# Optimization experiments

Hardware: AMD Instinct MI355X
Metric: run time of the kernel (lower is better)

Reference implementation:

```python
import jax, jax.numpy as jnp
import numpy as np

B, T, D, H, V, K = 64, 128, 300, 256, 30000, 16
FILTERS = [3, 4, 5]
FN = [100, 100, 100]
CLS = 5


def setup_inputs() -> dict:
    key = jax.random.key(0)
    ks = jax.random.split(key, 32)
    n = lambda i, shape, s=0.05: (jax.random.normal(ks[i], shape, jnp.float32) * s)
    inp = jax.random.randint(ks[0], (B, T), 0, V)
    emb = n(1, (V + 2, D)).at[V + 1].set(0.0)  # padding_idx row = 0
    # GRU (1 layer, bidirectional), PyTorch gate order r,z,n
    Wx_f, Wh_f = n(2, (3 * H, D)), n(3, (3 * H, H))
    bx_f, bh_f = n(4, (3 * H,)), n(5, (3 * H,))
    Wx_b, Wh_b = n(6, (3 * H, D)), n(7, (3 * H, H))
    bx_b, bh_b = n(8, (3 * H,)), n(9, (3 * H,))
    fc1c_W, fc1c_b = n(10, (D, 2 * H)), n(11, (D,))
    concept_table = n(12, (V, K, D), 0.1)
    counts = jax.random.randint(ks[13], (V,), 1, K + 1)
    concept_mask = (jnp.arange(K)[None, :] < counts[:, None])  # bool [V,K]
    conv_W0, conv_b0 = n(14, (FN[0], FILTERS[0] * 2 * D)), n(15, (FN[0],))
    conv_W1, conv_b1 = n(16, (FN[1], FILTERS[1] * 2 * D)), n(17, (FN[1],))
    conv_W2, conv_b2 = n(18, (FN[2], FILTERS[2] * 2 * D)), n(19, (FN[2],))
    fc1_W, fc1_b = n(20, (100, sum(FN))), n(21, (100,))
    fc2_W, fc2_b = n(22, (CLS, 100)), n(23, (CLS,))
    return dict(inp=inp, emb=emb, Wx_f=Wx_f, Wh_f=Wh_f, bx_f=bx_f, bh_f=bh_f,
                Wx_b=Wx_b, Wh_b=Wh_b, bx_b=bx_b, bh_b=bh_b,
                fc1c_W=fc1c_W, fc1c_b=fc1c_b,
                concept_table=concept_table, concept_mask=concept_mask,
                conv_W0=conv_W0, conv_b0=conv_b0, conv_W1=conv_W1, conv_b1=conv_b1,
                conv_W2=conv_W2, conv_b2=conv_b2,
                fc1_W=fc1_W, fc1_b=fc1_b, fc2_W=fc2_W, fc2_b=fc2_b)


def _gru_dir(x, Wx, Wh, bx, bh):
    # x: [B,T,D] -> hidden states [B,T,H]; PyTorch GRU cell math.
    xg = jnp.einsum('btd,gd->btg', x, Wx) + bx  # precompute input gates [B,T,3H]

    def step(h, xg_t):
        gh = h @ Wh.T + bh
        xr, xz, xn = jnp.split(xg_t, 3, axis=-1)
        hr, hz, hn = jnp.split(gh, 3, axis=-1)
        r = jax.nn.sigmoid(xr + hr)
        z = jax.nn.sigmoid(xz + hz)
        nn_ = jnp.tanh(xn + r * hn)
        h2 = (1.0 - z) * nn_ + z * h
        return h2, h2

    h0 = jnp.zeros((x.shape[0], Wh.shape[1]), x.dtype)
    _, ys = jax.lax.scan(step, h0, jnp.swapaxes(xg, 0, 1))
    return jnp.swapaxes(ys, 0, 1)


def _forward(inp, emb, Wx_f, Wh_f, bx_f, bh_f, Wx_b, Wh_b, bx_b, bh_b,
             fc1c_W, fc1c_b, concept_table, concept_mask,
             conv_W0, conv_b0, conv_W1, conv_b1, conv_W2, conv_b2,
             fc1_W, fc1_b, fc2_W, fc2_b):
    x = emb[inp]                                   # [B,T,D]
    hf = _gru_dir(x, Wx_f, Wh_f, bx_f, bh_f)
    hb = jnp.flip(_gru_dir(jnp.flip(x, 1), Wx_b, Wh_b, bx_b, bh_b), 1)
    out = jnp.concatenate([hf, hb], axis=-1)       # [B,T,2H]
    ctx = jnp.einsum('bth,dh->btd', out, fc1c_W) + fc1c_b  # [B,T,D] context
    # batched gather-attend-reduce over per-word concept lists
    conc = concept_table[inp]                      # [B,T,K,D]
    mask = concept_mask[inp]                       # [B,T,K] bool
    scores = jnp.einsum('btkd,btd->btk', conc, ctx)
    scores = jnp.where(mask, scores, jnp.float32(-1e30))
    attn = jax.nn.softmax(scores, axis=-1)
    concept = jnp.einsum('btk,btkd->btd', attn, conc)
    concept = jax.lax.stop_gradient(concept)       # original detaches via .data.numpy()
    feat = jnp.concatenate([ctx, concept], axis=-1)  # [B,T,2D]
    pooled = []
    for fs, W, b in ((FILTERS[0], conv_W0, conv_b0),
                     (FILTERS[1], conv_W1, conv_b1),
                     (FILTERS[2], conv_W2, conv_b2)):
        L = T - fs + 1
        # Conv1d(kernel=2D*fs, stride=2D) over flattened feat == token-window matmul
        win = jnp.concatenate([feat[:, i:i + L, :] for i in range(fs)], axis=-1)  # [B,L,fs*2D]
        c = jax.nn.relu(jnp.einsum('blk,fk->blf', win, W) + b)
        pooled.append(jnp.max(c, axis=1))          # max-pool over positions -> [B,FN]
    h = jnp.concatenate(pooled, axis=1)            # [B,300]; dropout is identity in eval
    h = h @ fc1_W.T + fc1_b
    h = h @ fc2_W.T + fc2_b
    return jax.nn.softmax(h, axis=1)


def reference(inp, emb, Wx_f, Wh_f, bx_f, bh_f, Wx_b, Wh_b, bx_b, bh_b,
              fc1c_W, fc1c_b, concept_table, concept_mask,
              conv_W0, conv_b0, conv_W1, conv_b1, conv_W2, conv_b2,
              fc1_W, fc1_b, fc2_W, fc2_b):
    return _forward(inp, emb, Wx_f, Wh_f, bx_f, bh_f, Wx_b, Wh_b, bx_b, bh_b,
                    fc1c_W, fc1c_b, concept_table, concept_mask,
                    conv_W0, conv_b0, conv_W1, conv_b1, conv_W2, conv_b2,
                    fc1_W, fc1_b, fc2_W, fc2_b)
```

## Files before the change

kernel.cpp:

```cpp
#include <hip/hip_runtime.h>


typedef unsigned short u16;
typedef unsigned int u32;
typedef __attribute__((ext_vector_type(4))) u16 u16x4;
typedef __attribute__((ext_vector_type(8))) u16 u16x8;
typedef __attribute__((ext_vector_type(8))) __bf16 bf16x8;
typedef __attribute__((ext_vector_type(4))) float f32x4;

__device__ __forceinline__ float bf2f(u16 u) {
    union { u32 i; float f; } x; x.i = ((u32)u) << 16; return x.f;
}
__device__ __forceinline__ u16 f2bf(float f) {
    union { float f; u32 i; } x; x.f = f;
    u32 r = x.i + 0x7FFFu + ((x.i >> 16) & 1u);
    return (u16)(r >> 16);
}
__device__ __forceinline__ float sigm(float x) { return 1.f / (1.f + __expf(-x)); }
__device__ __forceinline__ float tanh_(float x) {
    float e = __expf(-2.f * fabsf(x));
    float t = (1.f - e) / (1.f + e);
    return x < 0.f ? -t : t;
}

__global__ __launch_bounds__(256) void detect_k(
    const u32* __restrict__ cmask_raw, int* __restrict__ flags)
{
    __shared__ int cnt1;
    if (threadIdx.x == 0) cnt1 = 0;
    __syncthreads();
    int c1 = 0;
    for (int i = threadIdx.x; i < 1024; i += 256)
        if (cmask_raw[i] > 1u) c1++;
    if (c1) atomicAdd(&cnt1, c1);
    __syncthreads();
    if (threadIdx.x == 0) flags[1] = (cnt1 > 0) ? 1 : 0;
}

struct CvtDesc { const void* src; u16* dst; int n; };
struct CvtArgs { CvtDesc d[17]; };

__global__ __launch_bounds__(256) void convert_f32(CvtArgs a)
{
    CvtDesc de = a.d[blockIdx.y];
    int i4 = (blockIdx.x * 256 + threadIdx.x) * 4;
    if (i4 >= de.n) return;
    const float* s = (const float*)de.src + i4;
    if (i4 + 4 <= de.n) {
        u16x4 o; o[0] = f2bf(s[0]); o[1] = f2bf(s[1]); o[2] = f2bf(s[2]); o[3] = f2bf(s[3]);
        *(u16x4*)(de.dst + i4) = o;
    } else {
        for (int e = 0; e < 4 && i4 + e < de.n; ++e) de.dst[i4 + e] = f2bf(s[e]);
    }
}

__global__ __launch_bounds__(256) void build_mask(
    const void* __restrict__ cmask, int* __restrict__ mask16, const int* __restrict__ flags)
{
    int v = blockIdx.x * 256 + threadIdx.x;
    if (v >= 30000) return;
    int m = 0;
    if (flags[1]) {
        const unsigned char* p = (const unsigned char*)cmask + (size_t)v * 16;
#pragma unroll
        for (int k = 0; k < 16; ++k) if (p[k]) m |= (1 << k);
    } else {
        const int* p = (const int*)cmask + (size_t)v * 16;
#pragma unroll
        for (int k = 0; k < 16; ++k) if (p[k]) m |= (1 << k);
    }
    mask16[v] = m;
}

__global__ __launch_bounds__(256) void repack_conv(
    const float* __restrict__ cw0, const float* __restrict__ cw1,
    const float* __restrict__ cw2, u16* __restrict__ wcat)
{
    const int r = blockIdx.x;
    const int d0 = threadIdx.x * 4;
    if (d0 >= 600) return;
    const float* src;
    if (r < 300)      { int f = r % 100,       i = r / 100;        src = cw0 + (size_t)f * 1800 + i * 600; }
    else if (r < 700) { int rr = r - 300, f = rr % 100, i = rr / 100; src = cw1 + (size_t)f * 2400 + i * 600; }
    else              { int rr = r - 700, f = rr % 100, i = rr / 100; src = cw2 + (size_t)f * 3000 + i * 600; }
    float4 x = *(const float4*)(src + d0);
    u16x4 o; o[0] = f2bf(x.x); o[1] = f2bf(x.y); o[2] = f2bf(x.z); o[3] = f2bf(x.w);
    *(u16x4*)(wcat + (size_t)r * 600 + d0) = o;
}

template<int ROWMODE, int EPI, int OUTBF, int AF32>
__global__ __launch_bounds__(256) void gemm_bt(
    const void* __restrict__ Araw, const u16* __restrict__ W,
    const u16* __restrict__ bias, const int* __restrict__ rowidx,
    float* __restrict__ Cf, u16* __restrict__ Cb,
    int M, int N, int K, int lda, int ldc)
{
    __shared__ __align__(16) u16 sA[64 * 40];
    __shared__ __align__(16) u16 sW[64 * 40];

    const int tid = threadIdx.x;
    const int m0 = blockIdx.y * 64;
    const int n0 = blockIdx.x * 64;

    const int l  = tid & 63;
    const int w  = tid >> 6;
    const int wm = (w >> 1) << 5;
    const int wn = (w & 1) << 5;
    const int fr = l & 15;
    const int fk = (l >> 4) << 3;

    const int sr = tid >> 2;
    const int cb = (tid & 3) << 3;

    size_t abase;
    {
        int m = m0 + sr;
        if constexpr (ROWMODE == 1) abase = (size_t)rowidx[m] * (size_t)lda;
        else                        abase = (size_t)m * (size_t)lda;
    }
    const int  wrow   = n0 + sr;
    const bool wvalid = wrow < N;
    const size_t wbase = (size_t)wrow * (size_t)K;

    f32x4 acc00 = {0,0,0,0}, acc01 = {0,0,0,0}, acc10 = {0,0,0,0}, acc11 = {0,0,0,0};

    for (int k0 = 0; k0 < K; k0 += 32) {
        __syncthreads();
        {
            u16x4 v0 = {0,0,0,0}, v1 = {0,0,0,0};
            int k = k0 + cb;
            if constexpr (AF32) {
                const float* A = (const float*)Araw;
                if (k + 8 <= K) {
                    const float* p = A + abase + k;
                    float4 x0 = *(const float4*)p;
                    float4 x1 = *(const float4*)(p + 4);
                    v0[0] = f2bf(x0.x); v0[1] = f2bf(x0.y); v0[2] = f2bf(x0.z); v0[3] = f2bf(x0.w);
                    v1[0] = f2bf(x1.x); v1[1] = f2bf(x1.y); v1[2] = f2bf(x1.z); v1[3] = f2bf(x1.w);
                } else {
#pragma unroll
                    for (int e = 0; e < 4; ++e) { int kk = k + e;     if (kk < K) v0[e] = f2bf(A[abase + kk]); }
#pragma unroll
                    for (int e = 0; e < 4; ++e) { int kk = k + 4 + e; if (kk < K) v1[e] = f2bf(A[abase + kk]); }
                }
            } else {
                const u16* A = (const u16*)Araw;
                if (k + 8 <= K) {
                    const u16* p = A + abase + k;
                    v0 = *(const u16x4*)p;
                    v1 = *(const u16x4*)(p + 4);
                } else {
#pragma unroll
                    for (int e = 0; e < 4; ++e) { int kk = k + e;     if (kk < K) v0[e] = A[abase + kk]; }
#pragma unroll
                    for (int e = 0; e < 4; ++e) { int kk = k + 4 + e; if (kk < K) v1[e] = A[abase + kk]; }
                }
            }
            *(u16x4*)(sA + sr * 40 + cb)     = v0;
            *(u16x4*)(sA + sr * 40 + cb + 4) = v1;
        }
        {
            u16x4 v0 = {0,0,0,0}, v1 = {0,0,0,0};
            int k = k0 + cb;
            if (wvalid) {
                if (k + 8 <= K) {
                    const u16* p = W + wbase + k;
                    v0 = *(const u16x4*)p;
                    v1 = *(const u16x4*)(p + 4);
                } else {
#pragma unroll
                    for (int e = 0; e < 4; ++e) { int kk = k + e;     if (kk < K) v0[e] = W[wbase + kk]; }
#pragma unroll
                    for (int e = 0; e < 4; ++e) { int kk = k + 4 + e; if (kk < K) v1[e] = W[wbase + kk]; }
                }
            }
            *(u16x4*)(sW + sr * 40 + cb)     = v0;
            *(u16x4*)(sW + sr * 40 + cb + 4) = v1;
        }
        __syncthreads();

        bf16x8 a0 = *(const bf16x8*)(sA + (wm + fr)      * 40 + fk);
        bf16x8 a1 = *(const bf16x8*)(sA + (wm + 16 + fr) * 40 + fk);
        bf16x8 b0 = *(const bf16x8*)(sW + (wn + fr)      * 40 + fk);
        bf16x8 b1 = *(const bf16x8*)(sW + (wn + 16 + fr) * 40 + fk);

        acc00 = __builtin_amdgcn_mfma_f32_16x16x32_bf16(a0, b0, acc00, 0, 0, 0);
        acc01 = __builtin_amdgcn_mfma_f32_16x16x32_bf16(a0, b1, acc01, 0, 0, 0);
        acc10 = __builtin_amdgcn_mfma_f32_16x16x32_bf16(a1, b0, acc10, 0, 0, 0);
        acc11 = __builtin_amdgcn_mfma_f32_16x16x32_bf16(a1, b1, acc11, 0, 0, 0);
    }

    const int rb = (l >> 4) << 2;
    const int cc = l & 15;
#define EPILOG(ACC, I, J)                                                     \
    {                                                                         \
        int col = n0 + wn + (J)*16 + cc;                                      \
        if (col < N) {                                                        \
            float bv = (EPI >= 1) ? bf2f(bias[col]) : 0.f;                    \
            _Pragma("unroll")                                                 \
            for (int r = 0; r < 4; ++r) {                                     \
                int row = m0 + wm + (I)*16 + rb + r;                          \
                if (row < M) {                                                \
                    float v = ACC[r] + bv;                                    \
                    if (EPI == 2) v = fmaxf(v, 0.f);                          \
                    if (OUTBF) Cb[(size_t)row * ldc + col] = f2bf(v);         \
                    else       Cf[(size_t)row * ldc + col] = v;               \
                }                                                             \
            }                                                                 \
        }                                                                     \
    }
    EPILOG(acc00, 0, 0); EPILOG(acc01, 0, 1); EPILOG(acc10, 1, 0); EPILOG(acc11, 1, 1);
#undef EPILOG
}

#define GB 8
__global__ __launch_bounds__(512, 2) void gru_scan_mfma(
    const u16* __restrict__ xg,
    const u16* __restrict__ whf, const u16* __restrict__ whb,
    const u16* __restrict__ bhf, const u16* __restrict__ bhb,
    u16* __restrict__ outb)
{
    const int bg  = blockIdx.x;
    const int dir = blockIdx.y;
    const u16* wh = dir ? whb : whf;
    const u16* bh = dir ? bhb : bhf;

    const int tid = threadIdx.x;
    const int w = tid >> 6;
    const int l = tid & 63;

    __shared__ __align__(16) u16 h_bf[16][264];
    __shared__ __align__(16) float gh[GB][772];
    __shared__ float bh_s[768];

    for (int i = tid; i < 16 * 264; i += 512) ((u16*)h_bf)[i] = 0;
    for (int i = tid; i < 768; i += 512) bh_s[i] = bf2f(bh[i]);

    bf16x8 bfr[6][8];
#pragma unroll
    for (int c = 0; c < 6; ++c)
#pragma unroll
        for (int kt = 0; kt < 8; ++kt) {
            const int n = w * 96 + c * 16 + (l & 15);
            const int k = kt * 32 + (l >> 4) * 8;
            bfr[c][kt] = *(const bf16x8*)(wh + (size_t)n * 256 + k);
        }
#pragma unroll
    for (int c = 0; c < 6; ++c)
#pragma unroll
        for (int kt = 0; kt < 8; ++kt)
            asm volatile("" : "+v"(bfr[c][kt]));

    const int qrow = (l >> 4) << 2;
    const int arow = l & 15;
    const int aofs = (l >> 4) << 3;
    const int j0 = l * 4;
    const int bglob = bg * GB + w;
    f32x4 hreg = {0.f, 0.f, 0.f, 0.f};

    __syncthreads();

    for (int s = 0; s < 128; ++s) {
        const int t = dir ? (127 - s) : s;

        const size_t tb = (size_t)(bglob * 128 + t) * 1536 + dir * 768;
        u16x4 xr4 = *(const u16x4*)(xg + tb + j0);
        u16x4 xz4 = *(const u16x4*)(xg + tb + 256 + j0);
        u16x4 xn4 = *(const u16x4*)(xg + tb + 512 + j0);

        f32x4 acc[6];
#pragma unroll
        for (int c = 0; c < 6; ++c) acc[c] = (f32x4){0.f, 0.f, 0.f, 0.f};
#pragma unroll
        for (int kt = 0; kt < 8; ++kt) {
            bf16x8 a = *(const bf16x8*)(&h_bf[arow][kt * 32 + aofs]);
#pragma unroll
            for (int c = 0; c < 6; ++c)
                acc[c] = __builtin_amdgcn_mfma_f32_16x16x32_bf16(a, bfr[c][kt], acc[c], 0, 0, 0);
        }
        if (qrow < GB) {
#pragma unroll
            for (int c = 0; c < 6; ++c) {
                const int col = w * 96 + c * 16 + (l & 15);
#pragma unroll
                for (int r = 0; r < 4; ++r)
                    gh[qrow + r][col] = acc[c][r];
            }
        }
        __syncthreads();

        {
            f32x4 gr = *(const f32x4*)(&gh[w][j0]);
            f32x4 gz = *(const f32x4*)(&gh[w][256 + j0]);
            f32x4 gn = *(const f32x4*)(&gh[w][512 + j0]);
            f32x4 br = *(const f32x4*)(&bh_s[j0]);
            f32x4 bz = *(const f32x4*)(&bh_s[256 + j0]);
            f32x4 bn = *(const f32x4*)(&bh_s[512 + j0]);
            u16x4 ho;
#pragma unroll
            for (int e = 0; e < 4; ++e) {
                float r = sigm(bf2f(xr4[e]) + gr[e] + br[e]);
                float z = sigm(bf2f(xz4[e]) + gz[e] + bz[e]);
                float n = tanh_(bf2f(xn4[e]) + r * (gn[e] + bn[e]));
                float h2 = (1.f - z) * n + z * hreg[e];
                hreg[e] = h2;
                ho[e] = f2bf(h2);
            }
            *(u16x4*)(&h_bf[w][j0]) = ho;
            *(u16x4*)(outb + (size_t)(bglob * 128 + t) * 512 + dir * 256 + j0) = ho;
        }
        __syncthreads();
    }
}
#undef GB

__global__ __launch_bounds__(256) void attn_kernel(
    const int* __restrict__ inp, const float* __restrict__ ctab,
    const int* __restrict__ mask16, u16* __restrict__ feat)
{
    const int tok = blockIdx.x;
    const int tid = threadIdx.x;
    const int v = inp[tok];

    __shared__ float ctx_s[300];
    __shared__ __align__(16) u16 conc_s[16 * 300];
    __shared__ float sc_s[16];
    __shared__ float at_s[16];

    for (int d = tid; d < 300; d += 256) ctx_s[d] = bf2f(feat[(size_t)tok * 600 + d]);
    {
        const float4* src = (const float4*)(ctab + (size_t)v * 4800);
        for (int i = tid; i < 1200; i += 256) {
            float4 x = src[i];
            u16x4 o; o[0] = f2bf(x.x); o[1] = f2bf(x.y); o[2] = f2bf(x.z); o[3] = f2bf(x.w);
            *(u16x4*)(conc_s + i * 4) = o;
        }
    }
    __syncthreads();

    const int g = tid >> 4, ln = tid & 15;
    float s = 0.f;
    for (int d = ln; d < 300; d += 16) s += bf2f(conc_s[g * 300 + d]) * ctx_s[d];
    s += __shfl_xor(s, 1); s += __shfl_xor(s, 2); s += __shfl_xor(s, 4); s += __shfl_xor(s, 8);
    if (ln == 0) sc_s[g] = ((mask16[v] >> g) & 1) ? s : -1e30f;
    __syncthreads();

    if (tid == 0) {
        float m = -1e30f;
#pragma unroll
        for (int i = 0; i < 16; ++i) m = fmaxf(m, sc_s[i]);
        float p[16]; float den = 0.f;
#pragma unroll
        for (int i = 0; i < 16; ++i) {
            float pe = (sc_s[i] <= -1e29f) ? 0.f : __expf(sc_s[i] - m);
            p[i] = pe; den += pe;
        }
        float inv = den > 0.f ? 1.f / den : 0.f;
#pragma unroll
        for (int i = 0; i < 16; ++i) at_s[i] = p[i] * inv;
    }
    __syncthreads();

    for (int d = tid; d < 300; d += 256) {
        float a = 0.f;
#pragma unroll
        for (int g2 = 0; g2 < 16; ++g2) a += at_s[g2] * bf2f(conc_s[g2 * 300 + d]);
        feat[(size_t)tok * 600 + 300 + d] = f2bf(a);
    }
}

__global__ __launch_bounds__(128) void pool_fused(
    const u16* __restrict__ P, const u16* __restrict__ cbcat,
    float* __restrict__ pool)
{
    const int b = blockIdx.x, which = blockIdx.y, f = threadIdx.x;
    if (f >= 100) return;
    const int fs  = which == 0 ? 3 : (which == 1 ? 4 : 5);
    const int off = which == 0 ? 0 : (which == 1 ? 300 : 700);
    const int L   = 128 - fs + 1;
    const float bias = bf2f(cbcat[which * 100 + f]);
    float mm = -1e30f;
    for (int l2 = 0; l2 < L; ++l2) {
        float s = bias;
#pragma unroll 5
        for (int i = 0; i < fs; ++i)
            s += bf2f(P[(size_t)(b * 128 + l2 + i) * 1200 + off + i * 100 + f]);
        mm = fmaxf(mm, s);
    }
    pool[b * 300 + which * 100 + f] = fmaxf(mm, 0.f);
}

__global__ __launch_bounds__(128) void final_k(
    const float* __restrict__ pool,
    const u16* __restrict__ fc1W, const u16* __restrict__ fc1b,
    const u16* __restrict__ fc2W, const u16* __restrict__ fc2b,
    float* __restrict__ out)
{
    const int b = blockIdx.x, tid = threadIdx.x;
    __shared__ float ps[300], h1[100], lg[5];
    for (int d = tid; d < 300; d += 128) ps[d] = pool[b * 300 + d];
    __syncthreads();
    if (tid < 100) {
        float a = bf2f(fc1b[tid]);
        for (int k = 0; k < 300; ++k) a += bf2f(fc1W[tid * 300 + k]) * ps[k];
        h1[tid] = a;
    }
    __syncthreads();
    if (tid < 5) {
        float a = bf2f(fc2b[tid]);
        for (int k = 0; k < 100; ++k) a += bf2f(fc2W[tid * 100 + k]) * h1[k];
        lg[tid] = a;
    }
    __syncthreads();
    if (tid == 0) {
        float m = fmaxf(fmaxf(fmaxf(lg[0], lg[1]), fmaxf(lg[2], lg[3])), lg[4]);
        float e0 = __expf(lg[0] - m), e1 = __expf(lg[1] - m), e2 = __expf(lg[2] - m),
              e3 = __expf(lg[3] - m), e4 = __expf(lg[4] - m);
        float inv = 1.f / (e0 + e1 + e2 + e3 + e4);
        out[b * 5 + 0] = e0 * inv;
        out[b * 5 + 1] = e1 * inv;
        out[b * 5 + 2] = e2 * inv;
        out[b * 5 + 3] = e3 * inv;
        out[b * 5 + 4] = e4 * inv;
    }
}

extern "C" void kernel_launch(void* const* d_in, const int* in_sizes, int n_in,
                              void* d_out, int out_size, void* d_ws, size_t ws_size,
                              hipStream_t stream)
{
    (void)in_sizes; (void)n_in; (void)out_size; (void)ws_size;

    const int*  inp     = (const int*)d_in[0];
    const void* embR    = d_in[1];
    const void* WxfR    = d_in[2];
    const void* WhfR    = d_in[3];
    const void* bxfR    = d_in[4];
    const void* bhfR    = d_in[5];
    const void* WxbR    = d_in[6];
    const void* WhbR    = d_in[7];
    const void* bxbR    = d_in[8];
    const void* bhbR    = d_in[9];
    const void* fc1cWR  = d_in[10];
    const void* fc1cbR  = d_in[11];
    const void* ctabR   = d_in[12];
    const void* cmaskR  = d_in[13];
    const void* cw0R    = d_in[14];
    const void* cb0R    = d_in[15];
    const void* cw1R    = d_in[16];
    const void* cb1R    = d_in[17];
    const void* cw2R    = d_in[18];
    const void* cb2R    = d_in[19];
    const void* fc1WR   = d_in[20];
    const void* fc1bR   = d_in[21];
    const void* fc2WR   = d_in[22];
    const void* fc2bR   = d_in[23];

    char* ws = (char*)d_ws;
    size_t off = 0;
    auto alloc = [&](size_t bytes) -> char* {
        char* r = ws + off;
        off = (off + bytes + 255) & ~(size_t)255;
        return r;
    };

    u16*   xgc    = (u16*)alloc(8192ull * 1536 * 2);
    u16*   outb   = (u16*)alloc(8192ull * 512 * 2);
    u16*   feat   = (u16*)alloc(8192ull * 600 * 2);
    u16*   P      = (u16*)alloc(8192ull * 1200 * 2);
    float* pool   = (float*)alloc(64ull * 300 * 4);
    int*   flags  = (int*)alloc(256);
    int*   mask16 = (int*)alloc(30000ull * 4);
    u16*   wxcat  = (u16*)alloc(1536ull * 300 * 2);
    u16*   bxcat  = (u16*)alloc(1536ull * 2);
    u16*   whfc   = (u16*)alloc(196608ull * 2);
    u16*   whbc   = (u16*)alloc(196608ull * 2);
    u16*   bhfc   = (u16*)alloc(768ull * 2);
    u16*   bhbc   = (u16*)alloc(768ull * 2);
    u16*   fc1cWc = (u16*)alloc(153600ull * 2);
    u16*   fc1cbc = (u16*)alloc(300ull * 2);
    u16*   wcat   = (u16*)alloc(1200ull * 600 * 2);
    u16*   cbcat  = (u16*)alloc(300ull * 2);
    u16*   fc1Wc  = (u16*)alloc(30000ull * 2);
    u16*   fc1bc  = (u16*)alloc(100ull * 2);
    u16*   fc2Wc  = (u16*)alloc(500ull * 2);
    u16*   fc2bc  = (u16*)alloc(8ull * 2);

    detect_k<<<1, 256, 0, stream>>>((const u32*)cmaskR, flags);

    {
        CvtArgs a{};
        a.d[0]  = { WxfR,   wxcat,          230400 };
        a.d[1]  = { WxbR,   wxcat + 230400, 230400 };
        a.d[2]  = { bxfR,   bxcat,          768 };
        a.d[3]  = { bxbR,   bxcat + 768,    768 };
        a.d[4]  = { WhfR,   whfc,           196608 };
        a.d[5]  = { WhbR,   whbc,           196608 };
        a.d[6]  = { bhfR,   bhfc,           768 };
        a.d[7]  = { bhbR,   bhbc,           768 };
        a.d[8]  = { fc1cWR, fc1cWc,         153600 };
        a.d[9]  = { fc1cbR, fc1cbc,         300 };
        a.d[10] = { cb0R,   cbcat,          100 };
        a.d[11] = { cb1R,   cbcat + 100,    100 };
        a.d[12] = { cb2R,   cbcat + 200,    100 };
        a.d[13] = { fc1WR,  fc1Wc,          30000 };
        a.d[14] = { fc1bR,  fc1bc,          100 };
        a.d[15] = { fc2WR,  fc2Wc,          500 };
        a.d[16] = { fc2bR,  fc2bc,          5 };
        convert_f32<<<dim3(225, 17), 256, 0, stream>>>(a);
    }

    build_mask<<<118, 256, 0, stream>>>(cmaskR, mask16, flags);
    repack_conv<<<1200, 256, 0, stream>>>(
        (const float*)cw0R, (const float*)cw1R, (const float*)cw2R, wcat);

    gemm_bt<1, 1, 1, 1><<<dim3(24, 128), 256, 0, stream>>>(
        embR, wxcat, bxcat, inp, nullptr, xgc, 8192, 1536, 300, 300, 1536);

    gru_scan_mfma<<<dim3(8, 2), 512, 0, stream>>>(
        xgc, whfc, whbc, bhfc, bhbc, outb);

    gemm_bt<0, 1, 1, 0><<<dim3(5, 128), 256, 0, stream>>>(
        outb, fc1cWc, fc1cbc, nullptr, nullptr, feat, 8192, 300, 512, 512, 600);

    attn_kernel<<<dim3(8192), 256, 0, stream>>>(inp, (const float*)ctabR, mask16, feat);

    gemm_bt<0, 0, 1, 0><<<dim3(19, 128), 256, 0, stream>>>(
        feat, wcat, nullptr, nullptr, nullptr, P, 8192, 1200, 600, 600, 1200);

    pool_fused<<<dim3(64, 3), 128, 0, stream>>>(P, cbcat, pool);

    final_k<<<dim3(64), 128, 0, stream>>>(pool, fc1Wc, fc1bc, fc2Wc, fc2bc, (float*)d_out);
}
```

Before: 551.2 us.

## Add padded 128x128 MFMA GEMM with direct-to-LDS loads for input and conv GEMMs

Introduces a 128x128-tile bf16 MFMA GEMM that uses global_load_lds to copy tiles straight into LDS. It applies this GEMM to the GRU input projection and the conv-window GEMM, with operands zero-padded to K multiples of 32 (320 and 640) so there are no bounds branches. The embedding gather and fp32-to-bf16 conversion move into a separate staging kernel, and the r/z recurrent biases are folded into the input-projection bias so the GRU step does less work. The costs are extra staging kernels, a padded activation buffer, and wider feature rows.

```diff
diff --git a/kernel.cpp b/kernel.cpp
--- a/kernel.cpp
+++ b/kernel.cpp
@@ -22,6 +22,11 @@
     float t = (1.f - e) / (1.f + e);
     return x < 0.f ? -t : t;
 }
+__device__ __forceinline__ void gload16(const u16* g, u16* l) {
+    __builtin_amdgcn_global_load_lds(
+        (const __attribute__((address_space(1))) void*)g,
+        (__attribute__((address_space(3))) void*)l, 16, 0, 0);
+}
 
 __global__ __launch_bounds__(256) void detect_k(
     const u32* __restrict__ cmask_raw, int* __restrict__ flags)
@@ -38,7 +43,7 @@
 }
 
 struct CvtDesc { const void* src; u16* dst; int n; };
-struct CvtArgs { CvtDesc d[17]; };
+struct CvtArgs { CvtDesc d[11]; };
 
 __global__ __launch_bounds__(256) void convert_f32(CvtArgs a)
 {
@@ -78,21 +83,141 @@
 {
     const int r = blockIdx.x;
     const int d0 = threadIdx.x * 4;
-    if (d0 >= 600) return;
-    const float* src;
-    if (r < 300)      { int f = r % 100,       i = r / 100;        src = cw0 + (size_t)f * 1800 + i * 600; }
-    else if (r < 700) { int rr = r - 300, f = rr % 100, i = rr / 100; src = cw1 + (size_t)f * 2400 + i * 600; }
-    else              { int rr = r - 700, f = rr % 100, i = rr / 100; src = cw2 + (size_t)f * 3000 + i * 600; }
-    float4 x = *(const float4*)(src + d0);
-    u16x4 o; o[0] = f2bf(x.x); o[1] = f2bf(x.y); o[2] = f2bf(x.z); o[3] = f2bf(x.w);
-    *(u16x4*)(wcat + (size_t)r * 600 + d0) = o;
-}
-
-template<int ROWMODE, int EPI, int OUTBF, int AF32>
+    if (d0 >= 640) return;
+    u16x4 o = {0, 0, 0, 0};
+    if (r < 1200 && d0 < 600) {
+        const float* src;
+        if (r < 300)      { int f = r % 100,       i = r / 100;          src = cw0 + (size_t)f * 1800 + i * 600; }
+        else if (r < 700) { int rr = r - 300, f = rr % 100, i = rr / 100; src = cw1 + (size_t)f * 2400 + i * 600; }
+        else              { int rr = r - 700, f = rr % 100, i = rr / 100; src = cw2 + (size_t)f * 3000 + i * 600; }
+        float4 x = *(const float4*)(src + d0);
+        o[0] = f2bf(x.x); o[1] = f2bf(x.y); o[2] = f2bf(x.z); o[3] = f2bf(x.w);
+    }
+    *(u16x4*)(wcat + (size_t)r * 640 + d0) = o;
+}
+
+__global__ __launch_bounds__(64) void pack_wx(
+    const float* __restrict__ wxf, const float* __restrict__ wxb,
+    u16* __restrict__ wxpad)
+{
+    const int n = blockIdx.x;
+    const float* src = n < 768 ? wxf + (size_t)n * 300 : wxb + (size_t)(n - 768) * 300;
+    for (int c = threadIdx.x; c < 80; c += 64) {
+        u16x4 o = {0, 0, 0, 0};
+        if (c < 75) {
+            float4 x = *(const float4*)(src + c * 4);
+            o[0] = f2bf(x.x); o[1] = f2bf(x.y); o[2] = f2bf(x.z); o[3] = f2bf(x.w);
+        }
+        *(u16x4*)(wxpad + (size_t)n * 320 + c * 4) = o;
+    }
+}
+
+__global__ __launch_bounds__(256) void build_bias(
+    const float* __restrict__ bxf, const float* __restrict__ bhf,
+    const float* __restrict__ bxb, const float* __restrict__ bhb,
+    float* __restrict__ bias2)
+{
+    int c = blockIdx.x * 256 + threadIdx.x;
+    if (c >= 1536) return;
+    int cc = c < 768 ? c : c - 768;
+    const float* bx = c < 768 ? bxf : bxb;
+    const float* bh = c < 768 ? bhf : bhb;
+    float v = bx[cc];
+    if (cc < 512) v += bh[cc];
+    bias2[c] = v;
+}
+
+__global__ __launch_bounds__(64) void stage_x(
+    const int* __restrict__ inp, const float* __restrict__ emb,
+    u16* __restrict__ xstage)
+{
+    const int tok = blockIdx.x;
+    const float* src = emb + (size_t)inp[tok] * 300;
+    for (int c = threadIdx.x; c < 80; c += 64) {
+        u16x4 o = {0, 0, 0, 0};
+        if (c < 75) {
+            float4 x = *(const float4*)(src + c * 4);
+            o[0] = f2bf(x.x); o[1] = f2bf(x.y); o[2] = f2bf(x.z); o[3] = f2bf(x.w);
+        }
+        *(u16x4*)(xstage + (size_t)tok * 320 + c * 4) = o;
+    }
+}
+
+template<int EPI>
+__global__ __launch_bounds__(256) void gemm128(
+    const u16* __restrict__ A, const u16* __restrict__ W,
+    const float* __restrict__ bias, u16* __restrict__ C,
+    int Kpad, int Nout, int ldc)
+{
+    __shared__ __align__(16) u16 sA[128 * 32];
+    __shared__ __align__(16) u16 sW[128 * 32];
+
+    const int tid = threadIdx.x;
+    const int n0 = blockIdx.x * 128;
+    const int m0 = blockIdx.y * 128;
+
+    const int l  = tid & 63;
+    const int w  = tid >> 6;
+    const int wm = (w >> 1) << 6;
+    const int wn = (w & 1) << 6;
+    const int fr = l & 15;
+    const int fk = (l >> 4) << 3;
+
+    const int srow = tid >> 2;
+    const int scol = (tid & 3) << 3;
+
+    f32x4 acc[4][4];
+#pragma unroll
+    for (int i = 0; i < 4; ++i)
+#pragma unroll
+        for (int j = 0; j < 4; ++j) acc[i][j] = (f32x4){0.f, 0.f, 0.f, 0.f};
+
+    for (int k0 = 0; k0 < Kpad; k0 += 32) {
+        __syncthreads();
+#pragma unroll
+        for (int i = 0; i < 2; ++i) {
+            gload16(A + (size_t)(m0 + i * 64 + srow) * Kpad + k0 + scol,
+                    sA + i * 2048 + tid * 8);
+            gload16(W + (size_t)(n0 + i * 64 + srow) * Kpad + k0 + scol,
+                    sW + i * 2048 + tid * 8);
+        }
+        __syncthreads();
+
+        bf16x8 a[4], b[4];
+#pragma unroll
+        for (int i = 0; i < 4; ++i) {
+            a[i] = *(const bf16x8*)(sA + (wm + i * 16 + fr) * 32 + fk);
+            b[i] = *(const bf16x8*)(sW + (wn + i * 16 + fr) * 32 + fk);
+        }
+#pragma unroll
+        for (int i = 0; i < 4; ++i)
+#pragma unroll
+            for (int j = 0; j < 4; ++j)
+                acc[i][j] = __builtin_amdgcn_mfma_f32_16x16x32_bf16(a[i], b[j], acc[i][j], 0, 0, 0);
+    }
+
+    const int rb = (l >> 4) << 2;
+    const int cc = l & 15;
+#pragma unroll
+    for (int j = 0; j < 4; ++j) {
+        const int col = n0 + wn + j * 16 + cc;
+        if (col < Nout) {
+            const float bv = (EPI == 1) ? bias[col] : 0.f;
+#pragma unroll
+            for (int i = 0; i < 4; ++i) {
+#pragma unroll
+                for (int r = 0; r < 4; ++r) {
+                    const int row = m0 + wm + i * 16 + rb + r;
+                    C[(size_t)row * ldc + col] = f2bf(acc[i][j][r] + bv);
+                }
+            }
+        }
+    }
+}
+
 __global__ __launch_bounds__(256) void gemm_bt(
-    const void* __restrict__ Araw, const u16* __restrict__ W,
-    const u16* __restrict__ bias, const int* __restrict__ rowidx,
-    float* __restrict__ Cf, u16* __restrict__ Cb,
+    const u16* __restrict__ A, const u16* __restrict__ W,
+    const u16* __restrict__ bias, u16* __restrict__ Cb,
     int M, int N, int K, int lda, int ldc)
 {
     __shared__ __align__(16) u16 sA[64 * 40];
@@ -112,12 +237,7 @@
     const int sr = tid >> 2;
     const int cb = (tid & 3) << 3;
 
-    size_t abase;
-    {
-        int m = m0 + sr;
-        if constexpr (ROWMODE == 1) abase = (size_t)rowidx[m] * (size_t)lda;
-        else                        abase = (size_t)m * (size_t)lda;
-    }
+    const size_t abase = (size_t)(m0 + sr) * (size_t)lda;
     const int  wrow   = n0 + sr;
     const bool wvalid = wrow < N;
     const size_t wbase = (size_t)wrow * (size_t)K;
@@ -127,52 +247,16 @@
     for (int k0 = 0; k0 < K; k0 += 32) {
         __syncthreads();
         {
-            u16x4 v0 = {0,0,0,0}, v1 = {0,0,0,0};
-            int k = k0 + cb;
-            if constexpr (AF32) {
-                const float* A = (const float*)Araw;
-                if (k + 8 <= K) {
-                    const float* p = A + abase + k;
-                    float4 x0 = *(const float4*)p;
-                    float4 x1 = *(const float4*)(p + 4);
-                    v0[0] = f2bf(x0.x); v0[1] = f2bf(x0.y); v0[2] = f2bf(x0.z); v0[3] = f2bf(x0.w);
-                    v1[0] = f2bf(x1.x); v1[1] = f2bf(x1.y); v1[2] = f2bf(x1.z); v1[3] = f2bf(x1.w);
-                } else {
-#pragma unroll
-                    for (int e = 0; e < 4; ++e) { int kk = k + e;     if (kk < K) v0[e] = f2bf(A[abase + kk]); }
-#pragma unroll
-                    for (int e = 0; e < 4; ++e) { int kk = k + 4 + e; if (kk < K) v1[e] = f2bf(A[abase + kk]); }
-                }
-            } else {
-                const u16* A = (const u16*)Araw;
-                if (k + 8 <= K) {
-                    const u16* p = A + abase + k;
-                    v0 = *(const u16x4*)p;
-                    v1 = *(const u16x4*)(p + 4);
-                } else {
-#pragma unroll
-                    for (int e = 0; e < 4; ++e) { int kk = k + e;     if (kk < K) v0[e] = A[abase + kk]; }
-#pragma unroll
-                    for (int e = 0; e < 4; ++e) { int kk = k + 4 + e; if (kk < K) v1[e] = A[abase + kk]; }
-                }
-            }
-            *(u16x4*)(sA + sr * 40 + cb)     = v0;
-            *(u16x4*)(sA + sr * 40 + cb + 4) = v1;
+            const u16* p = A + abase + k0 + cb;
+            *(u16x4*)(sA + sr * 40 + cb)     = *(const u16x4*)p;
+            *(u16x4*)(sA + sr * 40 + cb + 4) = *(const u16x4*)(p + 4);
         }
         {
             u16x4 v0 = {0,0,0,0}, v1 = {0,0,0,0};
-            int k = k0 + cb;
             if (wvalid) {
-                if (k + 8 <= K) {
-                    const u16* p = W + wbase + k;
-                    v0 = *(const u16x4*)p;
-                    v1 = *(const u16x4*)(p + 4);
-                } else {
-#pragma unroll
-                    for (int e = 0; e < 4; ++e) { int kk = k + e;     if (kk < K) v0[e] = W[wbase + kk]; }
-#pragma unroll
-                    for (int e = 0; e < 4; ++e) { int kk = k + 4 + e; if (kk < K) v1[e] = W[wbase + kk]; }
-                }
+                const u16* p = W + wbase + k0 + cb;
+                v0 = *(const u16x4*)p;
+                v1 = *(const u16x4*)(p + 4);
             }
             *(u16x4*)(sW + sr * 40 + cb)     = v0;
             *(u16x4*)(sW + sr * 40 + cb + 4) = v1;
@@ -196,16 +280,12 @@
     {                                                                         \
         int col = n0 + wn + (J)*16 + cc;                                      \
         if (col < N) {                                                        \
-            float bv = (EPI >= 1) ? bf2f(bias[col]) : 0.f;                    \
+            float bv = bf2f(bias[col]);                                       \
             _Pragma("unroll")                                                 \
             for (int r = 0; r < 4; ++r) {                                     \
                 int row = m0 + wm + (I)*16 + rb + r;                          \
-                if (row < M) {                                                \
-                    float v = ACC[r] + bv;                                    \
-                    if (EPI == 2) v = fmaxf(v, 0.f);                          \
-                    if (OUTBF) Cb[(size_t)row * ldc + col] = f2bf(v);         \
-                    else       Cf[(size_t)row * ldc + col] = v;               \
-                }                                                             \
+                if (row < M)                                                  \
+                    Cb[(size_t)row * ldc + col] = f2bf(ACC[r] + bv);          \
             }                                                                 \
         }                                                                     \
     }
@@ -217,13 +297,13 @@
 __global__ __launch_bounds__(512, 2) void gru_scan_mfma(
     const u16* __restrict__ xg,
     const u16* __restrict__ whf, const u16* __restrict__ whb,
-    const u16* __restrict__ bhf, const u16* __restrict__ bhb,
+    const float* __restrict__ bhf, const float* __restrict__ bhb,
     u16* __restrict__ outb)
 {
     const int bg  = blockIdx.x;
     const int dir = blockIdx.y;
     const u16* wh = dir ? whb : whf;
-    const u16* bh = dir ? bhb : bhf;
+    const float* bh = dir ? bhb : bhf;
 
     const int tid = threadIdx.x;
     const int w = tid >> 6;
@@ -231,10 +311,8 @@
 
     __shared__ __align__(16) u16 h_bf[16][264];
     __shared__ __align__(16) float gh[GB][772];
-    __shared__ float bh_s[768];
 
     for (int i = tid; i < 16 * 264; i += 512) ((u16*)h_bf)[i] = 0;
-    for (int i = tid; i < 768; i += 512) bh_s[i] = bf2f(bh[i]);
 
     bf16x8 bfr[6][8];
 #pragma unroll
@@ -256,28 +334,30 @@
     const int aofs = (l >> 4) << 3;
     const int j0 = l * 4;
     const int bglob = bg * GB + w;
+    const float4 bhn4 = *(const float4*)(bh + 512 + j0);
     f32x4 hreg = {0.f, 0.f, 0.f, 0.f};
 
     __syncthreads();
 
     for (int s = 0; s < 128; ++s) {
         const int t = dir ? (127 - s) : s;
+
+        f32x4 acc[6];
+#pragma unroll
+        for (int c = 0; c < 6; ++c) acc[c] = (f32x4){0.f, 0.f, 0.f, 0.f};
+#pragma unroll
+        for (int kt = 0; kt < 8; ++kt) {
+            bf16x8 a = *(const bf16x8*)(&h_bf[arow][kt * 32 + aofs]);
+#pragma unroll
+            for (int c = 0; c < 6; ++c)
+                acc[c] = __builtin_amdgcn_mfma_f32_16x16x32_bf16(a, bfr[c][kt], acc[c], 0, 0, 0);
+        }
 
         const size_t tb = (size_t)(bglob * 128 + t) * 1536 + dir * 768;
         u16x4 xr4 = *(const u16x4*)(xg + tb + j0);
         u16x4 xz4 = *(const u16x4*)(xg + tb + 256 + j0);
         u16x4 xn4 = *(const u16x4*)(xg + tb + 512 + j0);
 
-        f32x4 acc[6];
-#pragma unroll
-        for (int c = 0; c < 6; ++c) acc[c] = (f32x4){0.f, 0.f, 0.f, 0.f};
-#pragma unroll
-        for (int kt = 0; kt < 8; ++kt) {
-            bf16x8 a = *(const bf16x8*)(&h_bf[arow][kt * 32 + aofs]);
-#pragma unroll
-            for (int c = 0; c < 6; ++c)
-                acc[c] = __builtin_amdgcn_mfma_f32_16x16x32_bf16(a, bfr[c][kt], acc[c], 0, 0, 0);
-        }
         if (qrow < GB) {
 #pragma unroll
             for (int c = 0; c < 6; ++c) {
@@ -289,26 +369,19 @@
         }
         __syncthreads();
 
-        {
-            f32x4 gr = *(const f32x4*)(&gh[w][j0]);
-            f32x4 gz = *(const f32x4*)(&gh[w][256 + j0]);
-            f32x4 gn = *(const f32x4*)(&gh[w][512 + j0]);
-            f32x4 br = *(const f32x4*)(&bh_s[j0]);
-            f32x4 bz = *(const f32x4*)(&bh_s[256 + j0]);
-            f32x4 bn = *(const f32x4*)(&bh_s[512 + j0]);
-            u16x4 ho;
-#pragma unroll
-            for (int e = 0; e < 4; ++e) {
-                float r = sigm(bf2f(xr4[e]) + gr[e] + br[e]);
-                float z = sigm(bf2f(xz4[e]) + gz[e] + bz[e]);
-                float n = tanh_(bf2f(xn4[e]) + r * (gn[e] + bn[e]));
-                float h2 = (1.f - z) * n + z * hreg[e];
-                hreg[e] = h2;
-                ho[e] = f2bf(h2);
-            }
-            *(u16x4*)(&h_bf[w][j0]) = ho;
-            *(u16x4*)(outb + (size_t)(bglob * 128 + t) * 512 + dir * 256 + j0) = ho;
-        }
+        u16x4 ho;
+#pragma unroll
+        for (int e = 0; e < 4; ++e) {
+            const int j = j0 + e;
+            float r = sigm(bf2f(xr4[e]) + gh[w][j]);
+            float z = sigm(bf2f(xz4[e]) + gh[w][256 + j]);
+            float n = tanh_(bf2f(xn4[e]) + r * (gh[w][512 + j] + bhn4[e]));
+            float h2 = (1.f - z) * n + z * hreg[e];
+            hreg[e] = h2;
+            ho[e] = f2bf(h2);
+        }
+        *(u16x4*)(&h_bf[w][j0]) = ho;
+        *(u16x4*)(outb + (size_t)(bglob * 128 + t) * 512 + dir * 256 + j0) = ho;
         __syncthreads();
     }
 }
@@ -327,7 +400,7 @@
     __shared__ float sc_s[16];
     __shared__ float at_s[16];
 
-    for (int d = tid; d < 300; d += 256) ctx_s[d] = bf2f(feat[(size_t)tok * 600 + d]);
+    for (int d = tid; d < 300; d += 256) ctx_s[d] = bf2f(feat[(size_t)tok * 640 + d]);
     {
         const float4* src = (const float4*)(ctab + (size_t)v * 4800);
         for (int i = tid; i < 1200; i += 256) {
@@ -361,11 +434,13 @@
     }
     __syncthreads();
 
-    for (int d = tid; d < 300; d += 256) {
+    for (int d = tid; d < 340; d += 256) {
         float a = 0.f;
-#pragma unroll
-        for (int g2 = 0; g2 < 16; ++g2) a += at_s[g2] * bf2f(conc_s[g2 * 300 + d]);
-        feat[(size_t)tok * 600 + 300 + d] = f2bf(a);
+        if (d < 300) {
+#pragma unroll
+            for (int g2 = 0; g2 < 16; ++g2) a += at_s[g2] * bf2f(conc_s[g2 * 300 + d]);
+        }
+        feat[(size_t)tok * 640 + 300 + d] = f2bf(a);
     }
 }
 
@@ -466,20 +541,19 @@
 
     u16*   xgc    = (u16*)alloc(8192ull * 1536 * 2);
     u16*   outb   = (u16*)alloc(8192ull * 512 * 2);
-    u16*   feat   = (u16*)alloc(8192ull * 600 * 2);
+    u16*   feat   = (u16*)alloc(8192ull * 640 * 2);
     u16*   P      = (u16*)alloc(8192ull * 1200 * 2);
+    u16*   xstage = (u16*)alloc(8192ull * 320 * 2);
     float* pool   = (float*)alloc(64ull * 300 * 4);
     int*   flags  = (int*)alloc(256);
     int*   mask16 = (int*)alloc(30000ull * 4);
-    u16*   wxcat  = (u16*)alloc(1536ull * 300 * 2);
-    u16*   bxcat  = (u16*)alloc(1536ull * 2);
+    u16*   wxpad  = (u16*)alloc(1536ull * 320 * 2);
+    float* bias2  = (float*)alloc(1536ull * 4);
     u16*   whfc   = (u16*)alloc(196608ull * 2);
     u16*   whbc   = (u16*)alloc(196608ull * 2);
-    u16*   bhfc   = (u16*)alloc(768ull * 2);
-    u16*   bhbc   = (u16*)alloc(768ull * 2);
     u16*   fc1cWc = (u16*)alloc(153600ull * 2);
     u16*   fc1cbc = (u16*)alloc(300ull * 2);
-    u16*   wcat   = (u16*)alloc(1200ull * 600 * 2);
+    u16*   wcat   = (u16*)alloc(1280ull * 640 * 2);
     u16*   cbcat  = (u16*)alloc(300ull * 2);
     u16*   fc1Wc  = (u16*)alloc(30000ull * 2);
     u16*   fc1bc  = (u16*)alloc(100ull * 2);
@@ -490,43 +564,41 @@
 
     {
         CvtArgs a{};
-        a.d[0]  = { WxfR,   wxcat,          230400 };
-        a.d[1]  = { WxbR,   wxcat + 230400, 230400 };
-        a.d[2]  = { bxfR,   bxcat,          768 };
-        a.d[3]  = { bxbR,   bxcat + 768,    768 };
-        a.d[4]  = { WhfR,   whfc,           196608 };
-        a.d[5]  = { WhbR,   whbc,           196608 };
-        a.d[6]  = { bhfR,   bhfc,           768 };
-        a.d[7]  = { bhbR,   bhbc,           768 };
-        a.d[8]  = { fc1cWR, fc1cWc,         153600 };
-        a.d[9]  = { fc1cbR, fc1cbc,         300 };
-        a.d[10] = { cb0R,   cbcat,          100 };
-        a.d[11] = { cb1R,   cbcat + 100,    100 };
-        a.d[12] = { cb2R,   cbcat + 200,    100 };
-        a.d[13] = { fc1WR,  fc1Wc,          30000 };
-        a.d[14] = { fc1bR,  fc1bc,          100 };
-        a.d[15] = { fc2WR,  fc2Wc,          500 };
-        a.d[16] = { fc2bR,  fc2bc,          5 };
-        convert_f32<<<dim3(225, 17), 256, 0, stream>>>(a);
+        a.d[0]  = { WhfR,   whfc,        196608 };
+        a.d[1]  = { WhbR,   whbc,        196608 };
+        a.d[2]  = { fc1cWR, fc1cWc,      153600 };
+        a.d[3]  = { fc1cbR, fc1cbc,      300 };
+        a.d[4]  = { cb0R,   cbcat,       100 };
+        a.d[5]  = { cb1R,   cbcat + 100, 100 };
+        a.d[6]  = { cb2R,   cbcat + 200, 100 };
+        a.d[7]  = { fc1WR,  fc1Wc,       30000 };
+        a.d[8]  = { fc1bR,  fc1bc,       100 };
+        a.d[9]  = { fc2WR,  fc2Wc,       500 };
+        a.d[10] = { fc2bR,  fc2bc,       5 };
+        convert_f32<<<dim3(192, 11), 256, 0, stream>>>(a);
     }
 
     build_mask<<<118, 256, 0, stream>>>(cmaskR, mask16, flags);
-    repack_conv<<<1200, 256, 0, stream>>>(
+    repack_conv<<<1280, 256, 0, stream>>>(
         (const float*)cw0R, (const float*)cw1R, (const float*)cw2R, wcat);
-
-    gemm_bt<1, 1, 1, 1><<<dim3(24, 128), 256, 0, stream>>>(
-        embR, wxcat, bxcat, inp, nullptr, xgc, 8192, 1536, 300, 300, 1536);
+    pack_wx<<<1536, 64, 0, stream>>>((const float*)WxfR, (const float*)WxbR, wxpad);
+    build_bias<<<6, 256, 0, stream>>>((const float*)bxfR, (const float*)bhfR,
+                                      (const float*)bxbR, (const float*)bhbR, bias2);
+    stage_x<<<8192, 64, 0, stream>>>(inp, (const float*)embR, xstage);
+
+    gemm128<1><<<dim3(12, 64), 256, 0, stream>>>(
+        xstage, wxpad, bias2, xgc, 320, 1536, 1536);
 
     gru_scan_mfma<<<dim3(8, 2), 512, 0, stream>>>(
-        xgc, whfc, whbc, bhfc, bhbc, outb);
-
-    gemm_bt<0, 1, 1, 0><<<dim3(5, 128), 256, 0, stream>>>(
-        outb, fc1cWc, fc1cbc, nullptr, nullptr, feat, 8192, 300, 512, 512, 600);
+        xgc, whfc, whbc, (const float*)bhfR, (const float*)bhbR, outb);
+
+    gemm_bt<<<dim3(5, 128), 256, 0, stream>>>(
+        outb, fc1cWc, fc1cbc, feat, 8192, 300, 512, 512, 640);
 
     attn_kernel<<<dim3(8192), 256, 0, stream>>>(inp, (const float*)ctabR, mask16, feat);
 
-    gemm_bt<0, 0, 1, 0><<<dim3(19, 128), 256, 0, stream>>>(
-        feat, wcat, nullptr, nullptr, nullptr, P, 8192, 1200, 600, 600, 1200);
+    gemm128<0><<<dim3(10, 64), 256, 0, stream>>>(
+        feat, wcat, nullptr, P, 640, 1200, 1200);
 
     pool_fused<<<dim3(64, 3), 128, 0, stream>>>(P, cbcat, pool);
 
```

Result: faster. 510.1 us (-7.4%).
